# Performance work log

Measured on AMD Instinct MI355X. Metric: run time of the kernel, lower is better.

Reference implementation:

```python
import jax, jax.numpy as jnp
import numpy as np

TEMPERATURE = 0.2
IOU_THRESHOLD = 0.0  # all proposals kept (keep mask is all-True); identical math, jit-friendly
M, K = 8192, 128
N_CLASSES = 60


def setup_inputs() -> dict:
    key = jax.random.key(0)
    k1, k2, k3 = jax.random.split(key, 3)
    features = jax.random.normal(k1, (M, K), dtype=jnp.float32)
    ious = jax.random.uniform(k2, (M,), dtype=jnp.float32)  # in [0,1) >= 0.0 threshold
    labels = jax.random.randint(k3, (M,), 0, N_CLASSES, dtype=jnp.int64)
    return {"features": features, "ious": ious, "labels": labels}


def reference(features, ious, labels):
    # keep = ious >= IOU_THRESHOLD is all-True by construction; no compaction needed.
    # L2-normalize features along feature dim (F.normalize, dim=1)
    f = features / jnp.linalg.norm(features, axis=1, keepdims=True)
    # [M, M] cosine similarity / temperature
    sim = jnp.matmul(f, f.T) / TEMPERATURE
    # row-max subtraction (detached in original)
    sim = sim - jax.lax.stop_gradient(jnp.max(sim, axis=1, keepdims=True))
    m = sim.shape[0]
    logits_mask = 1.0 - jnp.eye(m, dtype=sim.dtype)  # zero diagonal
    exp_sim = jnp.exp(sim) * logits_mask
    log_prob = sim - jnp.log(jnp.clip(jnp.sum(exp_sim, axis=1, keepdims=True), 1e-5))
    label_mask = (labels[:, None] == labels[None, :]).astype(sim.dtype)
    per_label_log_prob = jnp.sum(log_prob * logits_mask * label_mask, axis=1) / jnp.sum(label_mask, axis=1)
    loss = -per_label_log_prob
    coef = jnp.ones_like(ious)  # reweight_func='none' -> trivial
    return jnp.mean(loss * coef)
```

## Files before the change

### kernel.cpp

```cpp
#include <hip/hip_runtime.h>
#include <hip/hip_bf16.h>

#define M_ROWS 8192
#define K_DIM 128
#define NCLS 60
#define NPAN 32
#define NSIM 528
#define NSLAB 128

constexpr float SCL = 2.68579007f;
constexpr float LN2 = 0.69314718056f;

using f32x4 = __attribute__((ext_vector_type(4))) float;
using s16x8 = __attribute__((ext_vector_type(8))) short;

__device__ inline float bf2f(ushort u) {
    union { unsigned int i; float f; } v; v.i = ((unsigned int)u) << 16; return v.f;
}
__device__ inline float bfround(float x) {
    __hip_bfloat16 h = __float2bfloat16(x);
    return bf2f(*reinterpret_cast<const ushort*>(&h));
}
__device__ inline float fexp2(float x) {
#if __has_builtin(__builtin_amdgcn_exp2f)
    return __builtin_amdgcn_exp2f(x);
#else
    return exp2f(x);
#endif
}


__global__ __launch_bounds__(256) void kprep(const float* __restrict__ feat,
                                             const int* __restrict__ labels,
                                             ushort* __restrict__ fnr,
                                             ushort* __restrict__ fnp,
                                             float* __restrict__ slabS,
                                             float* __restrict__ slabC,
                                             float* __restrict__ out) {
    __shared__ ushort ln[16][128];
    __shared__ float Sl[NCLS * K_DIM];
    __shared__ float Cl[NCLS];
    __shared__ int lab[64];
    const int tid = threadIdx.x, wv = tid >> 6, lane = tid & 63;

    int row = wv * 4;
#pragma unroll
    for (int it = 0; it < 4; ++it, ++row) {
        const int grow = blockIdx.x * 16 + row;
        const float2 v = *(const float2*)&feat[(size_t)grow * K_DIM + lane * 2];
        float ss = v.x * v.x + v.y * v.y;
#pragma unroll
        for (int m = 1; m < 64; m <<= 1) ss += __shfl_xor(ss, m, 64);
        const float rs = rsqrtf(ss) * SCL;
        __hip_bfloat16 ha = __float2bfloat16(v.x * rs);
        __hip_bfloat16 hb = __float2bfloat16(v.y * rs);
        ushort2 o;
        o.x = *reinterpret_cast<const ushort*>(&ha);
        o.y = *reinterpret_cast<const ushort*>(&hb);
        *(ushort2*)&fnr[(size_t)grow * K_DIM + lane * 2] = o;
        *(ushort2*)&ln[row][lane * 2] = o;
    }
    __syncthreads();
    {
        const s16x8 vv = *(const s16x8*)&ln[tid & 15][(tid >> 4) * 8];
        *(s16x8*)&fnp[(size_t)blockIdx.x * 2048 + tid * 8] = vv;
    }
    if (blockIdx.x == 0 && tid == 0) out[0] = 0.f;

    if (blockIdx.x < NSLAB) {
        const int rbase = blockIdx.x * 64;
        for (int i = tid; i < NCLS * K_DIM; i += 256) Sl[i] = 0.f;
        if (tid < NCLS) Cl[tid] = 0.f;
        if (tid < 64) lab[tid] = labels[rbase + tid];
        __syncthreads();

        const int rsub = tid >> 4;
        const int kc = tid & 15;
#pragma unroll
        for (int it = 0; it < 4; ++it) {
            const int r = it * 16 + rsub;
            const int lb = lab[r];
            if (kc == 0) atomicAdd(&Cl[lb], 1.f);
            const f32x4 va = *(const f32x4*)&feat[(size_t)(rbase + r) * K_DIM + kc * 8];
            const f32x4 vb = *(const f32x4*)&feat[(size_t)(rbase + r) * K_DIM + kc * 8 + 4];
            float ss = va[0]*va[0] + va[1]*va[1] + va[2]*va[2] + va[3]*va[3]
                     + vb[0]*vb[0] + vb[1]*vb[1] + vb[2]*vb[2] + vb[3]*vb[3];
#pragma unroll
            for (int m = 1; m < 16; m <<= 1) ss += __shfl_xor(ss, m, 16);
            const float rs = rsqrtf(ss) * SCL;
            float* dst = &Sl[lb * K_DIM + kc * 8];
#pragma unroll
            for (int j = 0; j < 4; ++j) atomicAdd(&dst[j],     bfround(va[j] * rs));
#pragma unroll
            for (int j = 0; j < 4; ++j) atomicAdd(&dst[4 + j], bfround(vb[j] * rs));
        }
        __syncthreads();
        float* oS = slabS + (size_t)blockIdx.x * (NCLS * K_DIM);
        for (int i = tid; i < NCLS * K_DIM; i += 256) oS[i] = Sl[i];
        if (tid < NCLS) slabC[blockIdx.x * 64 + tid] = Cl[tid];
    }
}

__global__ __launch_bounds__(512) void kmain(const ushort* __restrict__ fnp,
                                             const float* __restrict__ slabS,
                                             const float* __restrict__ slabC,
                                             float* __restrict__ denomP,
                                             float* __restrict__ S,
                                             float* __restrict__ cntC) {
    __shared__ __align__(16) ushort ldsB[16 * 2048];
    __shared__ float colbuf[8][256];
    const int tid = threadIdx.x;
    const int lane = tid & 63;
    const int lrow = lane & 15;
    const int g = lane >> 4;
    const int wv = tid >> 6;

    const int bid = blockIdx.x;
    int I = (int)((65.0f - sqrtf(4225.0f - 8.0f * (float)bid)) * 0.5f);
    while ((I + 1) * 32 - ((I + 1) * I) / 2 <= bid) ++I;
    while (I * 32 - (I * (I - 1)) / 2 > bid) --I;
    const int J = I + (bid - (I * 32 - (I * (I - 1)) / 2));
    const bool offd = (J != I);
    const int rbase = I * 256 + wv * 32;

    {
        const ushort* gbase = fnp + (size_t)J * 16 * 2048;
#pragma unroll
        for (int it = 0; it < 8; ++it) {
            const int chunk = it * 512 + wv * 64;
            const ushort* src = gbase + (size_t)(chunk + lane) * 8;
            ushort* dst = &ldsB[(size_t)chunk * 8];
            __builtin_amdgcn_global_load_lds((const __attribute__((address_space(1))) void*)src,
                                             (__attribute__((address_space(3))) void*)dst, 16, 0, 0);
        }
    }

    s16x8 af[2][4];
#pragma unroll
    for (int m = 0; m < 2; ++m)
#pragma unroll
        for (int kk = 0; kk < 4; ++kk)
            af[m][kk] = *(const s16x8*)&fnp[(size_t)((rbase >> 4) + m) * 2048 + kk * 512 + lane * 8];

    __syncthreads();

    float pd[2][4] = {};

#pragma unroll
    for (int t = 0; t < 4; ++t) {
        f32x4 acc[2][4] = {};
#pragma unroll
        for (int kk = 0; kk < 4; ++kk) {
            s16x8 bfr[4];
#pragma unroll
            for (int n = 0; n < 4; ++n)
                bfr[n] = *(const s16x8*)&ldsB[(size_t)(t * 4 + n) * 2048 + kk * 512 + lane * 8];
#pragma unroll
            for (int m = 0; m < 2; ++m)
#pragma unroll
                for (int n = 0; n < 4; ++n)
                    acc[m][n] = __builtin_amdgcn_mfma_f32_16x16x32_bf16(af[m][kk], bfr[n], acc[m][n], 0, 0, 0);
        }
        float pcn[4] = {0.f, 0.f, 0.f, 0.f};
#pragma unroll
        for (int m = 0; m < 2; ++m)
#pragma unroll
            for (int n = 0; n < 4; ++n)
#pragma unroll
                for (int r = 0; r < 4; ++r) {
                    const float e = fexp2(acc[m][n][r]);
                    pd[m][r] += e;
                    pcn[n] += e;
                }
        if (offd) {
#pragma unroll
            for (int n = 0; n < 4; ++n) {
                float v = pcn[n];
                v += __shfl_xor(v, 16);
                v += __shfl_xor(v, 32);
                if (lane < 16) colbuf[wv][t * 64 + n * 16 + lrow] = v;
            }
        }
    }

#pragma unroll
    for (int m = 0; m < 2; ++m)
#pragma unroll
        for (int r = 0; r < 4; ++r) {
            float v = pd[m][r];
#pragma unroll
            for (int msk = 1; msk < 16; msk <<= 1) v += __shfl_xor(v, msk, 16);
            if (lrow == 0)
                denomP[(size_t)J * M_ROWS + rbase + m * 16 + g * 4 + r] = v;
        }

    if (offd) {
        __syncthreads();
        if (tid < 256) {
            float cv = 0.f;
#pragma unroll
            for (int w = 0; w < 8; ++w) cv += colbuf[w][tid];
            denomP[(size_t)I * M_ROWS + J * 256 + tid] = cv;
        }
    }

    if (bid < 31 && tid < 256) {
        const int i = bid * 256 + tid;
        if (i < NCLS * K_DIM) {
            float s = 0.f;
#pragma unroll 8
            for (int b = 0; b < NSLAB; ++b) s += slabS[(size_t)b * (NCLS * K_DIM) + i];
            S[i] = s;
        } else if (i < NCLS * K_DIM + NCLS) {
            const int c = i - NCLS * K_DIM;
            float s = 0.f;
#pragma unroll 8
            for (int b = 0; b < NSLAB; ++b) s += slabC[b * 64 + c];
            cntC[c] = s;
        }
    }
}

__global__ __launch_bounds__(1024) void kfin(const ushort* __restrict__ fn,
                                             const int* __restrict__ labels,
                                             const float* __restrict__ denomP,
                                             const float* __restrict__ S,
                                             const float* __restrict__ cntC,
                                             float* __restrict__ out) {
    const int tid = threadIdx.x;
    const int wv = tid >> 6, lane = tid & 63;
    const int row = blockIdx.x * 16 + wv;
    const ushort2 qv = *(const ushort2*)&fn[(size_t)row * K_DIM + lane * 2];
    const float f0 = bf2f(qv.x), f1 = bf2f(qv.y);
    const int c = labels[row];
    const float2 sv = *(const float2*)&S[c * K_DIM + lane * 2];
    float dot = f0 * sv.x + f1 * sv.y;
    float sii = f0 * f0 + f1 * f1;
#pragma unroll
    for (int msk = 1; msk < 64; msk <<= 1) {
        dot += __shfl_xor(dot, msk, 64);
        sii += __shfl_xor(sii, msk, 64);
    }
    float dsum = (lane < NPAN) ? denomP[(size_t)lane * M_ROWS + row] : 0.f;
#pragma unroll
    for (int msk = 1; msk < 32; msk <<= 1) dsum += __shfl_xor(dsum, msk, 32);

    __shared__ float ls[16];
    if (lane == 0) {
        const float cf = cntC[c];
        const float d = fmaxf(dsum - fexp2(sii), 1e-5f);
        const float p = (dot - sii) * LN2;
        ls[wv] = ((cf - 1.f) * __logf(d) - p) / cf;
    }
    __syncthreads();
    if (tid == 0) {
        float s = 0.f;
#pragma unroll
        for (int i = 0; i < 16; ++i) s += ls[i];
        atomicAdd(out, s * (1.0f / M_ROWS));
    }
}

extern "C" void kernel_launch(void* const* d_in, const int* in_sizes, int n_in,
                              void* d_out, int out_size, void* d_ws, size_t ws_size,
                              hipStream_t stream) {
    (void)in_sizes; (void)n_in; (void)out_size; (void)ws_size;
    const float* feat = (const float*)d_in[0];
    const int* labels = (const int*)d_in[2];
    float* out = (float*)d_out;
    char* ws = (char*)d_ws;
    ushort* fnr = (ushort*)ws;
    ushort* fnp = fnr + (size_t)M_ROWS * K_DIM;
    float* denomP = (float*)(fnp + (size_t)M_ROWS * K_DIM);
    float* S = denomP + (size_t)NPAN * M_ROWS;
    float* cntC = S + NCLS * K_DIM;
    float* slabS = cntC + 64;
    float* slabC = slabS + (size_t)NSLAB * NCLS * K_DIM;

    kprep<<<M_ROWS / 16, 256, 0, stream>>>(feat, labels, fnr, fnp, slabS, slabC, out);
    kmain<<<NSIM, 512, 0, stream>>>(fnp, slabS, slabC, denomP, S, cntC);
    kfin<<<M_ROWS / 16, 1024, 0, stream>>>(fnr, labels, denomP, S, cntC, out);
}
```

Measured before the change: 56.13 us.

## Split similarity tiles into half-panels and fold class-sum slabs into every prep block

The main kernel now launches twice as many blocks. Each block handles half of a 256-column panel (128 columns), so LDS use per block is halved and partial denominators go to 64 slots. The prep kernel processes 32 rows per block, and every block builds its per-class sum slab from the already-rounded bf16 values in LDS instead of re-reading the fp32 features. That gives 256 slabs. The final kernel sums all 64 denominator slots in one full-wave shuffle. This aims to improve occupancy and load balance across CUs. The cost is duplicated A-fragment loads and doubling the slab-reduction work in the main kernel's tail.

New measurement: 49.74 us. 11.4% less time.

```diff
diff --git a/kernel.cpp b/kernel.cpp
--- a/kernel.cpp
+++ b/kernel.cpp
@@ -4,9 +4,9 @@
 #define M_ROWS 8192
 #define K_DIM 128
 #define NCLS 60
-#define NPAN 32
+#define NSLOT 64
 #define NSIM 528
-#define NSLAB 128
+#define NSLAB 256
 
 constexpr float SCL = 2.68579007f;
 constexpr float LN2 = 0.69314718056f;
@@ -16,10 +16,6 @@
 
 __device__ inline float bf2f(ushort u) {
     union { unsigned int i; float f; } v; v.i = ((unsigned int)u) << 16; return v.f;
-}
-__device__ inline float bfround(float x) {
-    __hip_bfloat16 h = __float2bfloat16(x);
-    return bf2f(*reinterpret_cast<const ushort*>(&h));
 }
 __device__ inline float fexp2(float x) {
 #if __has_builtin(__builtin_amdgcn_exp2f)
@@ -37,16 +33,21 @@
                                              float* __restrict__ slabS,
                                              float* __restrict__ slabC,
                                              float* __restrict__ out) {
-    __shared__ ushort ln[16][128];
+    __shared__ __align__(16) ushort ln[32][128];
     __shared__ float Sl[NCLS * K_DIM];
     __shared__ float Cl[NCLS];
-    __shared__ int lab[64];
+    __shared__ int lab[32];
     const int tid = threadIdx.x, wv = tid >> 6, lane = tid & 63;
-
-    int row = wv * 4;
-#pragma unroll
-    for (int it = 0; it < 4; ++it, ++row) {
-        const int grow = blockIdx.x * 16 + row;
+    const int rbase = blockIdx.x * 32;
+
+    for (int i = tid; i < NCLS * K_DIM; i += 256) Sl[i] = 0.f;
+    if (tid < NCLS) Cl[tid] = 0.f;
+    if (tid < 32) lab[tid] = labels[rbase + tid];
+
+#pragma unroll
+    for (int it = 0; it < 8; ++it) {
+        const int r = wv * 8 + it;
+        const int grow = rbase + r;
         const float2 v = *(const float2*)&feat[(size_t)grow * K_DIM + lane * 2];
         float ss = v.x * v.x + v.y * v.y;
 #pragma unroll
@@ -58,47 +59,33 @@
         o.x = *reinterpret_cast<const ushort*>(&ha);
         o.y = *reinterpret_cast<const ushort*>(&hb);
         *(ushort2*)&fnr[(size_t)grow * K_DIM + lane * 2] = o;
-        *(ushort2*)&ln[row][lane * 2] = o;
-    }
-    __syncthreads();
-    {
-        const s16x8 vv = *(const s16x8*)&ln[tid & 15][(tid >> 4) * 8];
-        *(s16x8*)&fnp[(size_t)blockIdx.x * 2048 + tid * 8] = vv;
+        *(ushort2*)&ln[r][lane * 2] = o;
+    }
+    __syncthreads();
+
+#pragma unroll
+    for (int gb = 0; gb < 2; ++gb) {
+        const s16x8 vv = *(const s16x8*)&ln[gb * 16 + (tid & 15)][(tid >> 4) * 8];
+        *(s16x8*)&fnp[(size_t)(blockIdx.x * 2 + gb) * 2048 + tid * 8] = vv;
     }
     if (blockIdx.x == 0 && tid == 0) out[0] = 0.f;
 
-    if (blockIdx.x < NSLAB) {
-        const int rbase = blockIdx.x * 64;
-        for (int i = tid; i < NCLS * K_DIM; i += 256) Sl[i] = 0.f;
-        if (tid < NCLS) Cl[tid] = 0.f;
-        if (tid < 64) lab[tid] = labels[rbase + tid];
-        __syncthreads();
-
-        const int rsub = tid >> 4;
-        const int kc = tid & 15;
-#pragma unroll
-        for (int it = 0; it < 4; ++it) {
-            const int r = it * 16 + rsub;
-            const int lb = lab[r];
-            if (kc == 0) atomicAdd(&Cl[lb], 1.f);
-            const f32x4 va = *(const f32x4*)&feat[(size_t)(rbase + r) * K_DIM + kc * 8];
-            const f32x4 vb = *(const f32x4*)&feat[(size_t)(rbase + r) * K_DIM + kc * 8 + 4];
-            float ss = va[0]*va[0] + va[1]*va[1] + va[2]*va[2] + va[3]*va[3]
-                     + vb[0]*vb[0] + vb[1]*vb[1] + vb[2]*vb[2] + vb[3]*vb[3];
-#pragma unroll
-            for (int m = 1; m < 16; m <<= 1) ss += __shfl_xor(ss, m, 16);
-            const float rs = rsqrtf(ss) * SCL;
-            float* dst = &Sl[lb * K_DIM + kc * 8];
-#pragma unroll
-            for (int j = 0; j < 4; ++j) atomicAdd(&dst[j],     bfround(va[j] * rs));
-#pragma unroll
-            for (int j = 0; j < 4; ++j) atomicAdd(&dst[4 + j], bfround(vb[j] * rs));
-        }
-        __syncthreads();
-        float* oS = slabS + (size_t)blockIdx.x * (NCLS * K_DIM);
-        for (int i = tid; i < NCLS * K_DIM; i += 256) oS[i] = Sl[i];
-        if (tid < NCLS) slabC[blockIdx.x * 64 + tid] = Cl[tid];
-    }
+    const int rsub = tid >> 4;
+    const int kc = tid & 15;
+#pragma unroll
+    for (int it = 0; it < 2; ++it) {
+        const int r = it * 16 + rsub;
+        const int lb = lab[r];
+        if (kc == 0) atomicAdd(&Cl[lb], 1.f);
+        const s16x8 q = *(const s16x8*)&ln[r][kc * 8];
+        float* dst = &Sl[lb * K_DIM + kc * 8];
+#pragma unroll
+        for (int j = 0; j < 8; ++j) atomicAdd(&dst[j], bf2f((ushort)q[j]));
+    }
+    __syncthreads();
+    float* oS = slabS + (size_t)blockIdx.x * (NCLS * K_DIM);
+    for (int i = tid; i < NCLS * K_DIM; i += 256) oS[i] = Sl[i];
+    if (tid < NCLS) slabC[blockIdx.x * 64 + tid] = Cl[tid];
 }
 
 __global__ __launch_bounds__(512) void kmain(const ushort* __restrict__ fnp,
@@ -107,8 +94,8 @@
                                              float* __restrict__ denomP,
                                              float* __restrict__ S,
                                              float* __restrict__ cntC) {
-    __shared__ __align__(16) ushort ldsB[16 * 2048];
-    __shared__ float colbuf[8][256];
+    __shared__ __align__(16) ushort ldsB[8 * 2048];
+    __shared__ float colbuf[8][128];
     const int tid = threadIdx.x;
     const int lane = tid & 63;
     const int lrow = lane & 15;
@@ -116,17 +103,19 @@
     const int wv = tid >> 6;
 
     const int bid = blockIdx.x;
-    int I = (int)((65.0f - sqrtf(4225.0f - 8.0f * (float)bid)) * 0.5f);
-    while ((I + 1) * 32 - ((I + 1) * I) / 2 <= bid) ++I;
-    while (I * 32 - (I * (I - 1)) / 2 > bid) --I;
-    const int J = I + (bid - (I * 32 - (I * (I - 1)) / 2));
+    const int p = bid >> 1;
+    const int h = bid & 1;
+    int I = (int)((65.0f - sqrtf(4225.0f - 8.0f * (float)p)) * 0.5f);
+    while ((I + 1) * 32 - ((I + 1) * I) / 2 <= p) ++I;
+    while (I * 32 - (I * (I - 1)) / 2 > p) --I;
+    const int J = I + (p - (I * 32 - (I * (I - 1)) / 2));
     const bool offd = (J != I);
     const int rbase = I * 256 + wv * 32;
 
     {
-        const ushort* gbase = fnp + (size_t)J * 16 * 2048;
-#pragma unroll
-        for (int it = 0; it < 8; ++it) {
+        const ushort* gbase = fnp + (size_t)(J * 16 + h * 8) * 2048;
+#pragma unroll
+        for (int it = 0; it < 4; ++it) {
             const int chunk = it * 512 + wv * 64;
             const ushort* src = gbase + (size_t)(chunk + lane) * 8;
             ushort* dst = &ldsB[(size_t)chunk * 8];
@@ -147,7 +136,7 @@
     float pd[2][4] = {};
 
 #pragma unroll
-    for (int t = 0; t < 4; ++t) {
+    for (int t = 0; t < 2; ++t) {
         f32x4 acc[2][4] = {};
 #pragma unroll
         for (int kk = 0; kk < 4; ++kk) {
@@ -191,16 +180,17 @@
 #pragma unroll
             for (int msk = 1; msk < 16; msk <<= 1) v += __shfl_xor(v, msk, 16);
             if (lrow == 0)
-                denomP[(size_t)J * M_ROWS + rbase + m * 16 + g * 4 + r] = v;
+                denomP[(size_t)(2 * J + h) * M_ROWS + rbase + m * 16 + g * 4 + r] = v;
         }
 
     if (offd) {
         __syncthreads();
-        if (tid < 256) {
-            float cv = 0.f;
-#pragma unroll
-            for (int w = 0; w < 8; ++w) cv += colbuf[w][tid];
-            denomP[(size_t)I * M_ROWS + J * 256 + tid] = cv;
+        if (tid < 128) {
+            const float cv0 = colbuf[0][tid] + colbuf[1][tid] + colbuf[2][tid] + colbuf[3][tid];
+            const float cv1 = colbuf[4][tid] + colbuf[5][tid] + colbuf[6][tid] + colbuf[7][tid];
+            const size_t cpos = (size_t)J * 256 + h * 128 + tid;
+            denomP[(size_t)(2 * I) * M_ROWS + cpos] = cv0;
+            denomP[(size_t)(2 * I + 1) * M_ROWS + cpos] = cv1;
         }
     }
 
@@ -236,14 +226,13 @@
     const float2 sv = *(const float2*)&S[c * K_DIM + lane * 2];
     float dot = f0 * sv.x + f1 * sv.y;
     float sii = f0 * f0 + f1 * f1;
+    float dsum = denomP[(size_t)lane * M_ROWS + row];
 #pragma unroll
     for (int msk = 1; msk < 64; msk <<= 1) {
         dot += __shfl_xor(dot, msk, 64);
         sii += __shfl_xor(sii, msk, 64);
-    }
-    float dsum = (lane < NPAN) ? denomP[(size_t)lane * M_ROWS + row] : 0.f;
-#pragma unroll
-    for (int msk = 1; msk < 32; msk <<= 1) dsum += __shfl_xor(dsum, msk, 32);
+        dsum += __shfl_xor(dsum, msk, 64);
+    }
 
     __shared__ float ls[16];
     if (lane == 0) {
@@ -272,12 +261,12 @@
     ushort* fnr = (ushort*)ws;
     ushort* fnp = fnr + (size_t)M_ROWS * K_DIM;
     float* denomP = (float*)(fnp + (size_t)M_ROWS * K_DIM);
-    float* S = denomP + (size_t)NPAN * M_ROWS;
+    float* S = denomP + (size_t)NSLOT * M_ROWS;
     float* cntC = S + NCLS * K_DIM;
     float* slabS = cntC + 64;
     float* slabC = slabS + (size_t)NSLAB * NCLS * K_DIM;
 
-    kprep<<<M_ROWS / 16, 256, 0, stream>>>(feat, labels, fnr, fnp, slabS, slabC, out);
-    kmain<<<NSIM, 512, 0, stream>>>(fnp, slabS, slabC, denomP, S, cntC);
+    kprep<<<M_ROWS / 32, 256, 0, stream>>>(feat, labels, fnr, fnp, slabS, slabC, out);
+    kmain<<<NSIM * 2, 512, 0, stream>>>(fnp, slabS, slabC, denomP, S, cntC);
     kfin<<<M_ROWS / 16, 1024, 0, stream>>>(fnr, labels, denomP, S, cntC, out);
 }
```
